# Performance work log

Hardware: AMD Instinct MI355X
Metric: run time of the kernel (lower is better)

The kernel has to match this reference:

```python
import jax, jax.numpy as jnp
import numpy as np

LAMBDA_SCALE = 0.5
EPS = 1e-6

def setup_inputs() -> dict:
    key = jax.random.key(0)
    ks = jax.random.split(key, 9)
    B, S, D, E, F = 4, 2048, 1024, 8, 4096
    x = jax.random.normal(ks[0], (B, S, D), dtype=jnp.float32)
    prev_logits = jax.random.normal(ks[1], (B, S, E), dtype=jnp.float32)
    # router params (nn.Linear default init scale ~ 1/sqrt(fan_in))
    Wt = jax.random.normal(ks[2], (E, D), dtype=jnp.float32) / np.sqrt(D)
    Wgt = jax.random.normal(ks[3], (E, E), dtype=jnp.float32) / np.sqrt(E)
    We_logits = jnp.zeros((E,), dtype=jnp.float32)
    # expert MLPs, stacked over the expert axis
    W1 = jax.random.normal(ks[4], (E, D, F), dtype=jnp.float32) / np.sqrt(D)
    b1 = jax.random.normal(ks[5], (E, F), dtype=jnp.float32) * 0.01
    W2 = jax.random.normal(ks[6], (E, F, D), dtype=jnp.float32) / np.sqrt(F)
    b2 = jax.random.normal(ks[7], (E, D), dtype=jnp.float32) * 0.01
    return {"x": x, "prev_logits": prev_logits, "Wt": Wt, "Wgt": Wgt,
            "We_logits": We_logits, "W1": W1, "b1": b1, "W2": W2, "b2": b2}

def reference(x, prev_logits, Wt, Wgt, We_logits, W1, b1, W2, b2):
    # router logits: [B,S,E]
    logits = jnp.einsum('bsd,ed->bse', x, Wt) + jnp.einsum('bse,fe->bsf', prev_logits, Wgt)
    st = jax.nn.softmax(logits, axis=-1)
    We = jax.nn.sigmoid(We_logits)                      # [E]
    mask = (st > LAMBDA_SCALE * We).astype(st.dtype)    # data-dependent gate mask
    g = st * mask                                       # [B,S,E]
    # dense per-expert MLP over all tokens (faithful to the module)
    h = jax.nn.gelu(jnp.einsum('bsd,edf->bsef', x, W1) + b1, approximate=False)  # [B,S,E,F]
    outk = jnp.einsum('bsef,efd->bsed', h, W2) + b2     # [B,S,E,D]
    y = jnp.einsum('bse,bsed->bsd', g, outk)
    y = y / (jnp.sum(g, axis=-1, keepdims=True) + EPS)
    return (y, jax.lax.stop_gradient(logits))
```

## Files before the change

kernel.cpp:

```cpp
#include <hip/hip_runtime.h>
#include <math.h>

#define NTOK 8192
#define DDIM 1024
#define NEXP 8
#define FDIM 4096
#define MAXROWS 25600

typedef short bf16x8 __attribute__((ext_vector_type(8)));
typedef float f32x4 __attribute__((ext_vector_type(4)));

#define BAR() asm volatile("s_barrier" ::: "memory")
#define WAITVL0() asm volatile("s_waitcnt vmcnt(0) lgkmcnt(0)" ::: "memory")

static __device__ __forceinline__ unsigned short f2bf(float f) {
  unsigned int u = __float_as_uint(f);
  u += 0x7fffu + ((u >> 16) & 1u);
  return (unsigned short)(u >> 16);
}

static __device__ __forceinline__ void gl_lds16(const void* g, void* l) {
  __builtin_amdgcn_global_load_lds(
      (const __attribute__((address_space(1))) unsigned int*)g,
      (__attribute__((address_space(3))) unsigned int*)l, 16, 0, 0);
}

static __device__ __forceinline__ float gelu_f(float v) {
  float x2 = v * v;
  float p = fmaf(x2, 0.10294422f, 2.3021183f);
  float E = __builtin_amdgcn_exp2f(v * p);
  return v - v * __builtin_amdgcn_rcpf(E + 1.f);
}

__global__ __launch_bounds__(256) void router_kernel(
    const float* __restrict__ x, const float* __restrict__ prev,
    const float* __restrict__ Wt, const float* __restrict__ Wgt,
    const float* __restrict__ Wel,
    float* __restrict__ gn, float* __restrict__ logits_out)
{
  __shared__ float wt_s[NEXP * DDIM];
  const int tid = threadIdx.x;
  for (int i = tid; i < NEXP * DDIM; i += 256) wt_s[i] = Wt[i];
  __syncthreads();
  const int lane = tid & 63;
  const int t = blockIdx.x * 4 + (tid >> 6);

  const float* xr = x + (size_t)t * DDIM;
  float acc[NEXP];
#pragma unroll
  for (int e = 0; e < NEXP; ++e) acc[e] = 0.f;
  for (int k = lane; k < DDIM; k += 64) {
    float xv = xr[k];
#pragma unroll
    for (int e = 0; e < NEXP; ++e) acc[e] += xv * wt_s[e * DDIM + k];
  }
#pragma unroll
  for (int e = 0; e < NEXP; ++e) {
    float v = acc[e];
#pragma unroll
    for (int off = 32; off >= 1; off >>= 1) v += __shfl_xor(v, off);
    acc[e] = v;
  }
  float pl[NEXP];
#pragma unroll
  for (int e = 0; e < NEXP; ++e) pl[e] = prev[(size_t)t * NEXP + e];
#pragma unroll
  for (int e = 0; e < NEXP; ++e) {
    float s = acc[e];
#pragma unroll
    for (int e2 = 0; e2 < NEXP; ++e2) s += pl[e2] * Wgt[e * NEXP + e2];
    acc[e] = s;
  }
  float mx = acc[0];
#pragma unroll
  for (int e = 1; e < NEXP; ++e) mx = fmaxf(mx, acc[e]);
  float st[NEXP]; float se = 0.f;
#pragma unroll
  for (int e = 0; e < NEXP; ++e) { st[e] = expf(acc[e] - mx); se += st[e]; }
  float inv = 1.f / se;
  float g[NEXP]; float gs = 0.f;
#pragma unroll
  for (int e = 0; e < NEXP; ++e) {
    float s = st[e] * inv;
    float we = 1.f / (1.f + expf(-Wel[e]));
    float gg = (s > 0.5f * we) ? s : 0.f;
    g[e] = gg; gs += gg;
  }
  float r = 1.f / (gs + 1e-6f);
  if (lane < NEXP) {
    gn[(size_t)t * NEXP + lane] = g[lane] * r;
    logits_out[(size_t)t * NEXP + lane] = acc[lane];
  }
}

__global__ __launch_bounds__(256) void cast_kernel(
    const float* __restrict__ in, unsigned short* __restrict__ out)
{
  size_t i = ((size_t)blockIdx.x * 256 + threadIdx.x) * 8;
  float4 a = *(const float4*)(in + i);
  float4 b = *(const float4*)(in + i + 4);
  unsigned short tb[8];
  tb[0]=f2bf(a.x); tb[1]=f2bf(a.y); tb[2]=f2bf(a.z); tb[3]=f2bf(a.w);
  tb[4]=f2bf(b.x); tb[5]=f2bf(b.y); tb[6]=f2bf(b.z); tb[7]=f2bf(b.w);
  *(uint4*)(out + i) = *(const uint4*)tb;
}

__global__ __launch_bounds__(256) void count_kernel(
    const float* __restrict__ gn, int* __restrict__ cnt)
{
  const int e = blockIdx.x, tid = threadIdx.x;
  int c = 0;
  for (int t = tid; t < NTOK; t += 256) c += (gn[(size_t)t * NEXP + e] > 0.f) ? 1 : 0;
#pragma unroll
  for (int o = 32; o >= 1; o >>= 1) c += __shfl_xor(c, o);
  __shared__ int sm[4];
  if ((tid & 63) == 0) sm[tid >> 6] = c;
  __syncthreads();
  if (tid == 0) cnt[e] = sm[0] + sm[1] + sm[2] + sm[3];
}

__global__ __launch_bounds__(256) void compact_kernel(
    const float* __restrict__ gn, const int* __restrict__ cnt,
    int* __restrict__ offs, int* __restrict__ rowtok, int* __restrict__ rowof)
{
  const int e = blockIdx.x, tid = threadIdx.x;
  int base = 0;
#pragma unroll
  for (int q = 0; q < 8; ++q) if (q < e) base += (cnt[q] + 127) & ~127;
  const int padcnt = (cnt[e] + 127) & ~127;
  if (e == 0 && tid == 0) {
    int a = 0; offs[0] = 0;
#pragma unroll
    for (int q = 0; q < 8; ++q) { a += (cnt[q] + 127) & ~127; offs[q + 1] = a; }
  }
  __shared__ int wsm[4];
  __shared__ int running;
  if (tid == 0) running = 0;
  __syncthreads();
  const int lane = tid & 63, wv = tid >> 6;
  for (int c0 = 0; c0 < NTOK; c0 += 256) {
    const int t = c0 + tid;
    const bool pr = gn[(size_t)t * NEXP + e] > 0.f;
    unsigned long long bal = __ballot(pr);
    int pre = __popcll(bal & ((1ull << lane) - 1ull));
    if (lane == 0) wsm[wv] = __popcll(bal);
    __syncthreads();
    int wbase = 0;
#pragma unroll
    for (int q = 0; q < 4; ++q) if (q < wv) wbase += wsm[q];
    const int tot = wsm[0] + wsm[1] + wsm[2] + wsm[3];
    const int idx = base + running + wbase + pre;
    if (pr) rowtok[idx] = t;
    rowof[(size_t)t * NEXP + e] = pr ? idx : -1;
    __syncthreads();
    if (tid == 0) running += tot;
  }
  __syncthreads();
  for (int i = cnt[e] + tid; i < padcnt; i += 256) rowtok[base + i] = -1;
}

__global__ __launch_bounds__(256) void y_init_kernel(
    const float* __restrict__ gn, const float* __restrict__ b2,
    float* __restrict__ y)
{
  const int t = blockIdx.y;
  const int d = blockIdx.x * 256 + threadIdx.x;
  float s = 0.f;
#pragma unroll
  for (int e = 0; e < NEXP; ++e) s += gn[(size_t)t * NEXP + e] * b2[(size_t)e * DDIM + d];
  y[(size_t)t * DDIM + d] = s;
}

__global__ __launch_bounds__(256) void transcvt(
    const float* __restrict__ in, unsigned short* __restrict__ out,
    int Kin, int Nin)
{
  __shared__ float tile[64][65];
  const size_t zo = (size_t)blockIdx.z * Kin * Nin;
  const float* inp = in + zo;
  unsigned short* outp = out + zo;
  const int k0 = blockIdx.y * 64, n0 = blockIdx.x * 64;
  const int tid = threadIdx.x;
  const int r = tid >> 4, c4 = (tid & 15) * 4;
#pragma unroll
  for (int rr = 0; rr < 64; rr += 16) {
    float4 v = *(const float4*)(inp + (size_t)(k0 + r + rr) * Nin + n0 + c4);
    tile[r + rr][c4] = v.x; tile[r + rr][c4 + 1] = v.y;
    tile[r + rr][c4 + 2] = v.z; tile[r + rr][c4 + 3] = v.w;
  }
  __syncthreads();
#pragma unroll
  for (int it = 0; it < 2; ++it) {
    const int o = it * 256 + tid;
    const int n = o >> 3, ks = (o & 7) * 8;
    unsigned short tb[8];
#pragma unroll
    for (int j = 0; j < 8; ++j) tb[j] = f2bf(tile[ks + j][n]);
    *(uint4*)(outp + (size_t)(n0 + n) * Kin + k0 + ks) = *(const uint4*)tb;
  }
}


__global__ __launch_bounds__(128, 2) void gemm_h(
    const unsigned short* __restrict__ xb,
    const unsigned short* __restrict__ W,
    size_t wstride,
    const float* __restrict__ b1,
    const float* __restrict__ gn,
    const int* __restrict__ rowtok,
    const int* __restrict__ offs,
    int efix,
    unsigned short* __restrict__ hb)
{
  __shared__ unsigned short As[2][4096];
  __shared__ unsigned short Bs[2][4096];
  __shared__ float gns[128];
  __shared__ float b1s[128];
  __shared__ int toks[128];
  const int tid = threadIdx.x;

  int mt, e, hbase;
  if (efix >= 0) {
    e = efix;
    hbase = offs[e];
    mt = (hbase >> 7) + blockIdx.y;
    if (mt * 128 >= offs[e + 1]) return;
  } else {
    mt = blockIdx.y;
    const int r0 = mt * 128;
    if (r0 >= offs[8]) return;
    e = 0;
#pragma unroll
    for (int q = 1; q < 8; ++q) if (r0 >= offs[q]) e = q;
    hbase = 0;
  }
  const int n0 = blockIdx.x * 128;
  const unsigned short* We = W + (size_t)e * wstride;

  {
    const int tk = rowtok[mt * 128 + tid];
    toks[tid] = tk;
    gns[tid] = (tk >= 0) ? gn[(size_t)tk * NEXP + e] : 0.f;
    b1s[tid] = b1[(size_t)e * FDIM + n0 + tid];
  }
  __syncthreads();

  const int st_row = tid >> 2;
  const int st_off = (((tid & 3) ^ (st_row & 3)) << 3);
  const unsigned short* aP[4];
  const unsigned short* bP[4];
#pragma unroll
  for (int i = 0; i < 4; ++i) {
    int tk = toks[i * 32 + st_row]; if (tk < 0) tk = 0;
    aP[i] = xb + (size_t)tk * DDIM + st_off;
    bP[i] = We + (size_t)(n0 + i * 32 + st_row) * DDIM + st_off;
  }
  const int ldst = tid * 8;

  const int lane = tid & 63;
  const int w = tid >> 6;
  const int fr = lane & 15;
  const int rdoff = (((lane >> 4) ^ (lane & 3)) << 3);

  f32x4 acc[8][4];
#pragma unroll
  for (int i = 0; i < 8; ++i)
#pragma unroll
    for (int j = 0; j < 4; ++j) acc[i][j] = (f32x4){0.f, 0.f, 0.f, 0.f};

  auto stage = [&](int kt, int b) {
    const int ke = kt * 32;
#pragma unroll
    for (int i = 0; i < 4; ++i) {
      gl_lds16(aP[i] + ke, &As[b][i * 1024 + ldst]);
      gl_lds16(bP[i] + ke, &Bs[b][i * 1024 + ldst]);
    }
  };

  const int NT = DDIM / 32;
  stage(0, 0);
  WAITVL0(); BAR();

  for (int t = 0; t < NT; ++t) {
    const int cur = t & 1;
    if (t + 1 < NT) stage(t + 1, cur ^ 1);
    bf16x8 af[8], bfv[4];
#pragma unroll
    for (int i = 0; i < 8; ++i)
      af[i] = *(const bf16x8*)&As[cur][(i * 16 + fr) * 32 + rdoff];
#pragma unroll
    for (int j = 0; j < 4; ++j)
      bfv[j] = *(const bf16x8*)&Bs[cur][(w * 64 + j * 16 + fr) * 32 + rdoff];
#pragma unroll
    for (int i = 0; i < 8; ++i)
#pragma unroll
      for (int j = 0; j < 4; ++j)
        acc[i][j] = __builtin_amdgcn_mfma_f32_16x16x32_bf16(af[i], bfv[j], acc[i][j], 0, 0, 0);
    if (t + 1 < NT) { WAITVL0(); BAR(); }
  }

#pragma unroll
  for (int i = 0; i < 8; ++i)
#pragma unroll
    for (int r = 0; r < 4; ++r) {
      const int row = i * 16 + (lane >> 4) * 4 + r;
      const int tk = toks[row];
      if (tk < 0) continue;
      const float gv = gns[row];
      unsigned short* hrow = hb + (size_t)(mt * 128 + row - hbase) * FDIM + n0;
#pragma unroll
      for (int j = 0; j < 4; ++j) {
        const int col = w * 64 + j * 16 + fr;
        float v = gelu_f(acc[i][j][r] + b1s[col]) * gv;
        hrow[col] = f2bf(v);
      }
    }
}

__global__ __launch_bounds__(128, 2) void gemm_o(
    const unsigned short* __restrict__ hb,
    const unsigned short* __restrict__ W,
    size_t wstride,
    const int* __restrict__ rowtok,
    const int* __restrict__ offs,
    int efix,
    float* __restrict__ yout,
    int mode)
{
  __shared__ unsigned short As[2][4096];
  __shared__ unsigned short Bs[2][4096];
  __shared__ int toks[128];
  const int tid = threadIdx.x;

  int mt, e, hbase;
  if (efix >= 0) {
    e = efix;
    hbase = offs[e];
    mt = (hbase >> 7) + blockIdx.y;
    if (mt * 128 >= offs[e + 1]) return;
  } else {
    mt = blockIdx.y;
    const int r0 = mt * 128;
    if (r0 >= offs[8]) return;
    e = 0;
#pragma unroll
    for (int q = 1; q < 8; ++q) if (r0 >= offs[q]) e = q;
    hbase = 0;
  }
  const int n0 = blockIdx.x * 128;
  const unsigned short* We = W + (size_t)e * wstride;

  toks[tid] = rowtok[mt * 128 + tid];
  __syncthreads();

  const int st_row = tid >> 2;
  const int st_off = (((tid & 3) ^ (st_row & 3)) << 3);
  const unsigned short* aP[4];
  const unsigned short* bP[4];
#pragma unroll
  for (int i = 0; i < 4; ++i) {
    aP[i] = hb + (size_t)(mt * 128 - hbase + i * 32 + st_row) * FDIM + st_off;
    bP[i] = We + (size_t)(n0 + i * 32 + st_row) * FDIM + st_off;
  }
  const int ldst = tid * 8;

  const int lane = tid & 63;
  const int w = tid >> 6;
  const int fr = lane & 15;
  const int rdoff = (((lane >> 4) ^ (lane & 3)) << 3);

  f32x4 acc[8][4];
#pragma unroll
  for (int i = 0; i < 8; ++i)
#pragma unroll
    for (int j = 0; j < 4; ++j) acc[i][j] = (f32x4){0.f, 0.f, 0.f, 0.f};

  auto stage = [&](int kt, int b) {
    const int ke = kt * 32;
#pragma unroll
    for (int i = 0; i < 4; ++i) {
      gl_lds16(aP[i] + ke, &As[b][i * 1024 + ldst]);
      gl_lds16(bP[i] + ke, &Bs[b][i * 1024 + ldst]);
    }
  };

  const int NT = FDIM / 32;
  stage(0, 0);
  WAITVL0(); BAR();

  for (int t = 0; t < NT; ++t) {
    const int cur = t & 1;
    if (t + 1 < NT) stage(t + 1, cur ^ 1);
    bf16x8 af[8], bfv[4];
#pragma unroll
    for (int i = 0; i < 8; ++i)
      af[i] = *(const bf16x8*)&As[cur][(i * 16 + fr) * 32 + rdoff];
#pragma unroll
    for (int j = 0; j < 4; ++j)
      bfv[j] = *(const bf16x8*)&Bs[cur][(w * 64 + j * 16 + fr) * 32 + rdoff];
#pragma unroll
    for (int i = 0; i < 8; ++i)
#pragma unroll
      for (int j = 0; j < 4; ++j)
        acc[i][j] = __builtin_amdgcn_mfma_f32_16x16x32_bf16(af[i], bfv[j], acc[i][j], 0, 0, 0);
    if (t + 1 < NT) { WAITVL0(); BAR(); }
  }

#pragma unroll
  for (int i = 0; i < 8; ++i)
#pragma unroll
    for (int r = 0; r < 4; ++r) {
      const int row = i * 16 + (lane >> 4) * 4 + r;
      if (mode == 0) {
        const int tk = toks[row];
        if (tk < 0) continue;
        float* yrow = yout + (size_t)tk * DDIM + n0;
#pragma unroll
        for (int j = 0; j < 4; ++j) {
          const int col = w * 64 + j * 16 + fr;
          yrow[col] += acc[i][j][r];
        }
      } else {
        float* yrow = yout + (size_t)(mt * 128 + row) * DDIM + n0;
#pragma unroll
        for (int j = 0; j < 4; ++j) {
          const int col = w * 64 + j * 16 + fr;
          yrow[col] = acc[i][j][r];
        }
      }
    }
}

__global__ __launch_bounds__(256) void combine_kernel(
    const float* __restrict__ hb2, const int* __restrict__ rowof,
    const float* __restrict__ gn, const float* __restrict__ b2,
    float* __restrict__ y)
{
  const int t = blockIdx.y;
  const int d = blockIdx.x * 256 + threadIdx.x;
  float s = 0.f;
#pragma unroll
  for (int e = 0; e < NEXP; ++e) {
    s += gn[(size_t)t * NEXP + e] * b2[(size_t)e * DDIM + d];
    const int r = rowof[(size_t)t * NEXP + e];
    if (r >= 0) s += hb2[(size_t)r * DDIM + d];
  }
  y[(size_t)t * DDIM + d] = s;
}

extern "C" void kernel_launch(void* const* d_in, const int* in_sizes, int n_in,
                              void* d_out, int out_size, void* d_ws, size_t ws_size,
                              hipStream_t stream) {
  (void)in_sizes; (void)n_in; (void)out_size;
  const float* x    = (const float*)d_in[0];
  const float* prev = (const float*)d_in[1];
  const float* Wt   = (const float*)d_in[2];
  const float* Wgt  = (const float*)d_in[3];
  const float* Wel  = (const float*)d_in[4];
  const float* W1   = (const float*)d_in[5];
  const float* b1   = (const float*)d_in[6];
  const float* W2   = (const float*)d_in[7];
  const float* b2   = (const float*)d_in[8];

  float* y      = (float*)d_out;
  float* logits = y + (size_t)NTOK * DDIM;

  char* ws = (char*)d_ws;
  size_t pos = 0;
  auto take = [&](size_t bytes) -> char* {
    char* r = ws + pos; pos += (bytes + 255) & ~(size_t)255; return r;
  };
  float* gn            = (float*)take((size_t)NTOK * NEXP * 4);
  int* cnt             = (int*)take(64);
  int* offs            = (int*)take(64);
  int* rowtok          = (int*)take((size_t)MAXROWS * 4);
  int* rowof           = (int*)take((size_t)NTOK * NEXP * 4);
  unsigned short* xb   = (unsigned short*)take((size_t)NTOK * DDIM * 2);
  const size_t fixed = pos;

  const size_t wexp = (size_t)FDIM * DDIM;
  const size_t needA = fixed + 2 * NEXP * wexp * 2 + (size_t)MAXROWS * FDIM * 2
                       + (size_t)MAXROWS * DDIM * 4 + 4096;
  const bool tierA = ws_size >= needA;

  router_kernel<<<dim3(NTOK / 4), dim3(256), 0, stream>>>(x, prev, Wt, Wgt, Wel, gn, logits);
  cast_kernel<<<dim3((NTOK * DDIM) / (8 * 256)), dim3(256), 0, stream>>>(x, xb);
  count_kernel<<<dim3(NEXP), dim3(256), 0, stream>>>(gn, cnt);
  compact_kernel<<<dim3(NEXP), dim3(256), 0, stream>>>(gn, cnt, offs, rowtok, rowof);

  if (tierA) {
    unsigned short* W1b = (unsigned short*)take(NEXP * wexp * 2);
    unsigned short* W2b = (unsigned short*)take(NEXP * wexp * 2);
    unsigned short* hb  = (unsigned short*)take((size_t)MAXROWS * FDIM * 2);
    float* hb2          = (float*)take((size_t)MAXROWS * DDIM * 4);

    transcvt<<<dim3(FDIM / 64, DDIM / 64, NEXP), dim3(256), 0, stream>>>(W1, W1b, DDIM, FDIM);
    transcvt<<<dim3(DDIM / 64, FDIM / 64, NEXP), dim3(256), 0, stream>>>(W2, W2b, FDIM, DDIM);
    gemm_h<<<dim3(FDIM / 128, MAXROWS / 128), dim3(128), 0, stream>>>(
        xb, W1b, wexp, b1, gn, rowtok, offs, -1, hb);
    gemm_o<<<dim3(DDIM / 128, MAXROWS / 128), dim3(128), 0, stream>>>(
        hb, W2b, wexp, rowtok, offs, -1, hb2, 1);
    combine_kernel<<<dim3(DDIM / 256, NTOK), dim3(256), 0, stream>>>(hb2, rowof, gn, b2, y);
  } else {
    unsigned short* Wb = (unsigned short*)take(wexp * 2);
    unsigned short* hb = (unsigned short*)take((size_t)NTOK * FDIM * 2);

    y_init_kernel<<<dim3(DDIM / 256, NTOK), dim3(256), 0, stream>>>(gn, b2, y);
    for (int e = 0; e < NEXP; ++e) {
      transcvt<<<dim3(FDIM / 64, DDIM / 64, 1), dim3(256), 0, stream>>>(
          W1 + (size_t)e * wexp, Wb, DDIM, FDIM);
      gemm_h<<<dim3(FDIM / 128, 64), dim3(128), 0, stream>>>(
          xb, Wb, 0, b1, gn, rowtok, offs, e, hb);
      transcvt<<<dim3(DDIM / 64, FDIM / 64, 1), dim3(256), 0, stream>>>(
          W2 + (size_t)e * wexp, Wb, FDIM, DDIM);
      gemm_o<<<dim3(DDIM / 128, 64), dim3(128), 0, stream>>>(
          hb, Wb, 0, rowtok, offs, e, y, 0);
    }
  }
}
```

Before: 546.4 us.

## Use 256x256-tile, 512-thread grouped GEMMs with interleaved prefetch and bf16 expert outputs

Replaces the 128x128 grouped expert GEMMs on the main path with 256x256 tiles, K=64 steps and 8 waves. Global-to-LDS loads for the next tile are split into chunks interleaved with MFMA groups, using partial vmcnt waits and s_setprio. Expert padding goes to 256 rows to match the new tiles. The second GEMM's per-expert outputs are stored as bf16 instead of fp32, halving intermediate traffic for the combine step. This raises per-block LDS and register use, adds padded rows, and loses some precision in the intermediate outputs.

Measured after the change: 500.9 us, median of 3. 1.09x faster.

```diff
diff --git a/kernel.cpp b/kernel.cpp
--- a/kernel.cpp
+++ b/kernel.cpp
@@ -5,18 +5,21 @@
 #define DDIM 1024
 #define NEXP 8
 #define FDIM 4096
-#define MAXROWS 25600
+#define MAXROWS 26624
 
 typedef short bf16x8 __attribute__((ext_vector_type(8)));
 typedef float f32x4 __attribute__((ext_vector_type(4)));
 
 #define BAR() asm volatile("s_barrier" ::: "memory")
-#define WAITVL0() asm volatile("s_waitcnt vmcnt(0) lgkmcnt(0)" ::: "memory")
+#define WAITV(n) asm volatile("s_waitcnt vmcnt(" #n ")" ::: "memory")
 
 static __device__ __forceinline__ unsigned short f2bf(float f) {
   unsigned int u = __float_as_uint(f);
   u += 0x7fffu + ((u >> 16) & 1u);
   return (unsigned short)(u >> 16);
+}
+static __device__ __forceinline__ float bf2f(unsigned short b) {
+  return __uint_as_float(((unsigned int)b) << 16);
 }
 
 static __device__ __forceinline__ void gl_lds16(const void* g, void* l) {
@@ -126,12 +129,12 @@
   const int e = blockIdx.x, tid = threadIdx.x;
   int base = 0;
 #pragma unroll
-  for (int q = 0; q < 8; ++q) if (q < e) base += (cnt[q] + 127) & ~127;
-  const int padcnt = (cnt[e] + 127) & ~127;
+  for (int q = 0; q < 8; ++q) if (q < e) base += (cnt[q] + 255) & ~255;
+  const int padcnt = (cnt[e] + 255) & ~255;
   if (e == 0 && tid == 0) {
     int a = 0; offs[0] = 0;
 #pragma unroll
-    for (int q = 0; q < 8; ++q) { a += (cnt[q] + 127) & ~127; offs[q + 1] = a; }
+    for (int q = 0; q < 8; ++q) { a += (cnt[q] + 255) & ~255; offs[q + 1] = a; }
   }
   __shared__ int wsm[4];
   __shared__ int running;
@@ -201,10 +204,362 @@
 }
 
 
-__global__ __launch_bounds__(128, 2) void gemm_h(
+__global__ __launch_bounds__(512, 2) void gemm_h256(
     const unsigned short* __restrict__ xb,
     const unsigned short* __restrict__ W,
-    size_t wstride,
+    const float* __restrict__ b1,
+    const float* __restrict__ gn,
+    const int* __restrict__ rowtok,
+    const int* __restrict__ offs,
+    unsigned short* __restrict__ hb)
+{
+  __shared__ unsigned short As[2][256 * 64];
+  __shared__ unsigned short Bs[2][256 * 64];
+  __shared__ float gns[256];
+  __shared__ float b1s[256];
+  __shared__ int toks[256];
+  const int tid = threadIdx.x;
+  const int r0 = blockIdx.y * 256;
+  if (r0 >= offs[8]) return;
+  int e = 0;
+#pragma unroll
+  for (int q = 1; q < 8; ++q) if (r0 >= offs[q]) e = q;
+  const int n0 = blockIdx.x * 256;
+  const unsigned short* We = W + (size_t)e * FDIM * DDIM;
+
+  if (tid < 256) {
+    const int tk = rowtok[r0 + tid];
+    toks[tid] = tk;
+    gns[tid] = (tk >= 0) ? gn[(size_t)tk * NEXP + e] : 0.f;
+    b1s[tid] = b1[(size_t)e * FDIM + n0 + tid];
+  }
+  __syncthreads();
+
+  const int rc = tid >> 3;
+  const int gld = tid & 7;
+  const int gsrc = gld ^ (rc & 7);
+  const unsigned short* aP[4];
+  const unsigned short* bP[4];
+#pragma unroll
+  for (int c = 0; c < 4; ++c) {
+    int tk = toks[c * 64 + rc]; if (tk < 0) tk = 0;
+    aP[c] = xb + (size_t)tk * DDIM + gsrc * 8;
+    bP[c] = We + (size_t)(n0 + c * 64 + rc) * DDIM + gsrc * 8;
+  }
+
+  const int lane = tid & 63;
+  const int wid = tid >> 6;
+  const int wm = (wid >> 2) * 128;
+  const int wn = (wid & 3) * 64;
+  const int fr = lane & 15;
+  const int q4 = lane >> 4;
+
+  f32x4 acc[8][4];
+#pragma unroll
+  for (int i = 0; i < 8; ++i)
+#pragma unroll
+    for (int j = 0; j < 4; ++j) acc[i][j] = (f32x4){0.f, 0.f, 0.f, 0.f};
+
+  auto stA = [&](int kt, int b, int c) { gl_lds16(aP[c] + kt * 64, &As[b][c * 4096 + tid * 8]); };
+  auto stB = [&](int kt, int b, int c) { gl_lds16(bP[c] + kt * 64, &Bs[b][c * 4096 + tid * 8]); };
+  auto rdA = [&](int cur, int i, int kk) -> bf16x8 {
+    const int row = wm + i * 16 + fr;
+    const int sl = (kk * 4 + q4) ^ (row & 7);
+    return *(const bf16x8*)&As[cur][row * 64 + sl * 8];
+  };
+  auto rdB = [&](int cur, int j, int kk) -> bf16x8 {
+    const int row = wn + j * 16 + fr;
+    const int sl = (kk * 4 + q4) ^ (row & 7);
+    return *(const bf16x8*)&Bs[cur][row * 64 + sl * 8];
+  };
+
+  const int NT = DDIM / 64;
+  bf16x8 aX[4][2], aY[4][2], bb[2][2];
+
+#pragma unroll
+  for (int c = 0; c < 4; ++c) { stA(0, 0, c); stB(0, 0, c); }
+  WAITV(0); BAR();
+
+  for (int t = 0; t < NT - 1; ++t) {
+    const int cur = t & 1, nxt = cur ^ 1;
+    stA(t + 1, nxt, 0); stA(t + 1, nxt, 1);
+    WAITV(2); BAR();
+#pragma unroll
+    for (int i = 0; i < 4; ++i) { aX[i][0] = rdA(cur, i, 0); aX[i][1] = rdA(cur, i, 1); }
+#pragma unroll
+    for (int j = 0; j < 2; ++j) { bb[j][0] = rdB(cur, j, 0); bb[j][1] = rdB(cur, j, 1); }
+    __builtin_amdgcn_s_setprio(1);
+#pragma unroll
+    for (int i = 0; i < 4; ++i)
+#pragma unroll
+      for (int j = 0; j < 2; ++j)
+#pragma unroll
+        for (int kk = 0; kk < 2; ++kk)
+          acc[i][j] = __builtin_amdgcn_mfma_f32_16x16x32_bf16(aX[i][kk], bb[j][kk], acc[i][j], 0, 0, 0);
+    __builtin_amdgcn_s_setprio(0);
+    stA(t + 1, nxt, 2); stA(t + 1, nxt, 3);
+#pragma unroll
+    for (int i = 0; i < 4; ++i) { aY[i][0] = rdA(cur, 4 + i, 0); aY[i][1] = rdA(cur, 4 + i, 1); }
+    __builtin_amdgcn_s_setprio(1);
+#pragma unroll
+    for (int i = 0; i < 4; ++i)
+#pragma unroll
+      for (int j = 0; j < 2; ++j)
+#pragma unroll
+        for (int kk = 0; kk < 2; ++kk)
+          acc[4 + i][j] = __builtin_amdgcn_mfma_f32_16x16x32_bf16(aY[i][kk], bb[j][kk], acc[4 + i][j], 0, 0, 0);
+    __builtin_amdgcn_s_setprio(0);
+    stB(t + 1, nxt, 0); stB(t + 1, nxt, 1);
+#pragma unroll
+    for (int j = 0; j < 2; ++j) { bb[j][0] = rdB(cur, 2 + j, 0); bb[j][1] = rdB(cur, 2 + j, 1); }
+    __builtin_amdgcn_s_setprio(1);
+#pragma unroll
+    for (int i = 0; i < 4; ++i)
+#pragma unroll
+      for (int j = 0; j < 2; ++j)
+#pragma unroll
+        for (int kk = 0; kk < 2; ++kk)
+          acc[4 + i][2 + j] = __builtin_amdgcn_mfma_f32_16x16x32_bf16(aY[i][kk], bb[j][kk], acc[4 + i][2 + j], 0, 0, 0);
+    __builtin_amdgcn_s_setprio(0);
+    stB(t + 1, nxt, 2); stB(t + 1, nxt, 3);
+    __builtin_amdgcn_s_setprio(1);
+#pragma unroll
+    for (int i = 0; i < 4; ++i)
+#pragma unroll
+      for (int j = 0; j < 2; ++j)
+#pragma unroll
+        for (int kk = 0; kk < 2; ++kk)
+          acc[i][2 + j] = __builtin_amdgcn_mfma_f32_16x16x32_bf16(aX[i][kk], bb[j][kk], acc[i][2 + j], 0, 0, 0);
+    __builtin_amdgcn_s_setprio(0);
+    BAR();
+  }
+  {
+    const int cur = (NT - 1) & 1;
+    WAITV(0); BAR();
+#pragma unroll
+    for (int i = 0; i < 4; ++i) { aX[i][0] = rdA(cur, i, 0); aX[i][1] = rdA(cur, i, 1); }
+#pragma unroll
+    for (int i = 0; i < 4; ++i) { aY[i][0] = rdA(cur, 4 + i, 0); aY[i][1] = rdA(cur, 4 + i, 1); }
+#pragma unroll
+    for (int j = 0; j < 2; ++j) { bb[j][0] = rdB(cur, j, 0); bb[j][1] = rdB(cur, j, 1); }
+#pragma unroll
+    for (int i = 0; i < 4; ++i)
+#pragma unroll
+      for (int j = 0; j < 2; ++j)
+#pragma unroll
+        for (int kk = 0; kk < 2; ++kk) {
+          acc[i][j] = __builtin_amdgcn_mfma_f32_16x16x32_bf16(aX[i][kk], bb[j][kk], acc[i][j], 0, 0, 0);
+          acc[4 + i][j] = __builtin_amdgcn_mfma_f32_16x16x32_bf16(aY[i][kk], bb[j][kk], acc[4 + i][j], 0, 0, 0);
+        }
+#pragma unroll
+    for (int j = 0; j < 2; ++j) { bb[j][0] = rdB(cur, 2 + j, 0); bb[j][1] = rdB(cur, 2 + j, 1); }
+#pragma unroll
+    for (int i = 0; i < 4; ++i)
+#pragma unroll
+      for (int j = 0; j < 2; ++j)
+#pragma unroll
+        for (int kk = 0; kk < 2; ++kk) {
+          acc[i][2 + j] = __builtin_amdgcn_mfma_f32_16x16x32_bf16(aX[i][kk], bb[j][kk], acc[i][2 + j], 0, 0, 0);
+          acc[4 + i][2 + j] = __builtin_amdgcn_mfma_f32_16x16x32_bf16(aY[i][kk], bb[j][kk], acc[4 + i][2 + j], 0, 0, 0);
+        }
+  }
+
+#pragma unroll
+  for (int i = 0; i < 8; ++i)
+#pragma unroll
+    for (int rr = 0; rr < 4; ++rr) {
+      const int row = wm + i * 16 + q4 * 4 + rr;
+      const int tk = toks[row];
+      if (tk < 0) continue;
+      const float gv = gns[row];
+      unsigned short* hrow = hb + (size_t)(r0 + row) * FDIM + n0;
+#pragma unroll
+      for (int j = 0; j < 4; ++j) {
+        const int col = wn + j * 16 + fr;
+        hrow[col] = f2bf(gelu_f(acc[i][j][rr] + b1s[col]) * gv);
+      }
+    }
+}
+
+__global__ __launch_bounds__(512, 2) void gemm_o256(
+    const unsigned short* __restrict__ hb,
+    const unsigned short* __restrict__ W,
+    const int* __restrict__ offs,
+    unsigned short* __restrict__ hb2)
+{
+  __shared__ unsigned short As[2][256 * 64];
+  __shared__ unsigned short Bs[2][256 * 64];
+  const int tid = threadIdx.x;
+  const int r0 = blockIdx.y * 256;
+  if (r0 >= offs[8]) return;
+  int e = 0;
+#pragma unroll
+  for (int q = 1; q < 8; ++q) if (r0 >= offs[q]) e = q;
+  const int n0 = blockIdx.x * 256;
+  const unsigned short* We = W + (size_t)e * FDIM * DDIM;
+
+  const int rc = tid >> 3;
+  const int gld = tid & 7;
+  const int gsrc = gld ^ (rc & 7);
+  const unsigned short* aP[4];
+  const unsigned short* bP[4];
+#pragma unroll
+  for (int c = 0; c < 4; ++c) {
+    aP[c] = hb + (size_t)(r0 + c * 64 + rc) * FDIM + gsrc * 8;
+    bP[c] = We + (size_t)(n0 + c * 64 + rc) * FDIM + gsrc * 8;
+  }
+
+  const int lane = tid & 63;
+  const int wid = tid >> 6;
+  const int wm = (wid >> 2) * 128;
+  const int wn = (wid & 3) * 64;
+  const int fr = lane & 15;
+  const int q4 = lane >> 4;
+
+  f32x4 acc[8][4];
+#pragma unroll
+  for (int i = 0; i < 8; ++i)
+#pragma unroll
+    for (int j = 0; j < 4; ++j) acc[i][j] = (f32x4){0.f, 0.f, 0.f, 0.f};
+
+  auto stA = [&](int kt, int b, int c) { gl_lds16(aP[c] + kt * 64, &As[b][c * 4096 + tid * 8]); };
+  auto stB = [&](int kt, int b, int c) { gl_lds16(bP[c] + kt * 64, &Bs[b][c * 4096 + tid * 8]); };
+  auto rdA = [&](int cur, int i, int kk) -> bf16x8 {
+    const int row = wm + i * 16 + fr;
+    const int sl = (kk * 4 + q4) ^ (row & 7);
+    return *(const bf16x8*)&As[cur][row * 64 + sl * 8];
+  };
+  auto rdB = [&](int cur, int j, int kk) -> bf16x8 {
+    const int row = wn + j * 16 + fr;
+    const int sl = (kk * 4 + q4) ^ (row & 7);
+    return *(const bf16x8*)&Bs[cur][row * 64 + sl * 8];
+  };
+
+  const int NT = FDIM / 64;
+  bf16x8 aX[4][2], aY[4][2], bb[2][2];
+
+#pragma unroll
+  for (int c = 0; c < 4; ++c) { stA(0, 0, c); stB(0, 0, c); }
+  WAITV(0); BAR();
+
+  for (int t = 0; t < NT - 1; ++t) {
+    const int cur = t & 1, nxt = cur ^ 1;
+    stA(t + 1, nxt, 0); stA(t + 1, nxt, 1);
+    WAITV(2); BAR();
+#pragma unroll
+    for (int i = 0; i < 4; ++i) { aX[i][0] = rdA(cur, i, 0); aX[i][1] = rdA(cur, i, 1); }
+#pragma unroll
+    for (int j = 0; j < 2; ++j) { bb[j][0] = rdB(cur, j, 0); bb[j][1] = rdB(cur, j, 1); }
+    __builtin_amdgcn_s_setprio(1);
+#pragma unroll
+    for (int i = 0; i < 4; ++i)
+#pragma unroll
+      for (int j = 0; j < 2; ++j)
+#pragma unroll
+        for (int kk = 0; kk < 2; ++kk)
+          acc[i][j] = __builtin_amdgcn_mfma_f32_16x16x32_bf16(aX[i][kk], bb[j][kk], acc[i][j], 0, 0, 0);
+    __builtin_amdgcn_s_setprio(0);
+    stA(t + 1, nxt, 2); stA(t + 1, nxt, 3);
+#pragma unroll
+    for (int i = 0; i < 4; ++i) { aY[i][0] = rdA(cur, 4 + i, 0); aY[i][1] = rdA(cur, 4 + i, 1); }
+    __builtin_amdgcn_s_setprio(1);
+#pragma unroll
+    for (int i = 0; i < 4; ++i)
+#pragma unroll
+      for (int j = 0; j < 2; ++j)
+#pragma unroll
+        for (int kk = 0; kk < 2; ++kk)
+          acc[4 + i][j] = __builtin_amdgcn_mfma_f32_16x16x32_bf16(aY[i][kk], bb[j][kk], acc[4 + i][j], 0, 0, 0);
+    __builtin_amdgcn_s_setprio(0);
+    stB(t + 1, nxt, 0); stB(t + 1, nxt, 1);
+#pragma unroll
+    for (int j = 0; j < 2; ++j) { bb[j][0] = rdB(cur, 2 + j, 0); bb[j][1] = rdB(cur, 2 + j, 1); }
+    __builtin_amdgcn_s_setprio(1);
+#pragma unroll
+    for (int i = 0; i < 4; ++i)
+#pragma unroll
+      for (int j = 0; j < 2; ++j)
+#pragma unroll
+        for (int kk = 0; kk < 2; ++kk)
+          acc[4 + i][2 + j] = __builtin_amdgcn_mfma_f32_16x16x32_bf16(aY[i][kk], bb[j][kk], acc[4 + i][2 + j], 0, 0, 0);
+    __builtin_amdgcn_s_setprio(0);
+    stB(t + 1, nxt, 2); stB(t + 1, nxt, 3);
+    __builtin_amdgcn_s_setprio(1);
+#pragma unroll
+    for (int i = 0; i < 4; ++i)
+#pragma unroll
+      for (int j = 0; j < 2; ++j)
+#pragma unroll
+        for (int kk = 0; kk < 2; ++kk)
+          acc[i][2 + j] = __builtin_amdgcn_mfma_f32_16x16x32_bf16(aX[i][kk], bb[j][kk], acc[i][2 + j], 0, 0, 0);
+    __builtin_amdgcn_s_setprio(0);
+    BAR();
+  }
+  {
+    const int cur = (NT - 1) & 1;
+    WAITV(0); BAR();
+#pragma unroll
+    for (int i = 0; i < 4; ++i) { aX[i][0] = rdA(cur, i, 0); aX[i][1] = rdA(cur, i, 1); }
+#pragma unroll
+    for (int i = 0; i < 4; ++i) { aY[i][0] = rdA(cur, 4 + i, 0); aY[i][1] = rdA(cur, 4 + i, 1); }
+#pragma unroll
+    for (int j = 0; j < 2; ++j) { bb[j][0] = rdB(cur, j, 0); bb[j][1] = rdB(cur, j, 1); }
+#pragma unroll
+    for (int i = 0; i < 4; ++i)
+#pragma unroll
+      for (int j = 0; j < 2; ++j)
+#pragma unroll
+        for (int kk = 0; kk < 2; ++kk) {
+          acc[i][j] = __builtin_amdgcn_mfma_f32_16x16x32_bf16(aX[i][kk], bb[j][kk], acc[i][j], 0, 0, 0);
+          acc[4 + i][j] = __builtin_amdgcn_mfma_f32_16x16x32_bf16(aY[i][kk], bb[j][kk], acc[4 + i][j], 0, 0, 0);
+        }
+#pragma unroll
+    for (int j = 0; j < 2; ++j) { bb[j][0] = rdB(cur, 2 + j, 0); bb[j][1] = rdB(cur, 2 + j, 1); }
+#pragma unroll
+    for (int i = 0; i < 4; ++i)
+#pragma unroll
+      for (int j = 0; j < 2; ++j)
+#pragma unroll
+        for (int kk = 0; kk < 2; ++kk) {
+          acc[i][2 + j] = __builtin_amdgcn_mfma_f32_16x16x32_bf16(aX[i][kk], bb[j][kk], acc[i][2 + j], 0, 0, 0);
+          acc[4 + i][2 + j] = __builtin_amdgcn_mfma_f32_16x16x32_bf16(aY[i][kk], bb[j][kk], acc[4 + i][2 + j], 0, 0, 0);
+        }
+  }
+
+#pragma unroll
+  for (int i = 0; i < 8; ++i)
+#pragma unroll
+    for (int rr = 0; rr < 4; ++rr) {
+      const int row = wm + i * 16 + q4 * 4 + rr;
+      unsigned short* orow = hb2 + (size_t)(r0 + row) * DDIM + n0;
+#pragma unroll
+      for (int j = 0; j < 4; ++j) {
+        const int col = wn + j * 16 + fr;
+        orow[col] = f2bf(acc[i][j][rr]);
+      }
+    }
+}
+
+__global__ __launch_bounds__(256) void combine_kernel(
+    const unsigned short* __restrict__ hb2, const int* __restrict__ rowof,
+    const float* __restrict__ gn, const float* __restrict__ b2,
+    float* __restrict__ y)
+{
+  const int t = blockIdx.y;
+  const int d = blockIdx.x * 256 + threadIdx.x;
+  float s = 0.f;
+#pragma unroll
+  for (int e = 0; e < NEXP; ++e) {
+    s += gn[(size_t)t * NEXP + e] * b2[(size_t)e * DDIM + d];
+    const int r = rowof[(size_t)t * NEXP + e];
+    if (r >= 0) s += bf2f(hb2[(size_t)r * DDIM + d]);
+  }
+  y[(size_t)t * DDIM + d] = s;
+}
+
+__global__ __launch_bounds__(128, 2) void gemm_h128(
+    const unsigned short* __restrict__ xb,
+    const unsigned short* __restrict__ W,
     const float* __restrict__ b1,
     const float* __restrict__ gn,
     const int* __restrict__ rowtok,
@@ -218,24 +573,12 @@
   __shared__ float b1s[128];
   __shared__ int toks[128];
   const int tid = threadIdx.x;
-
-  int mt, e, hbase;
-  if (efix >= 0) {
-    e = efix;
-    hbase = offs[e];
-    mt = (hbase >> 7) + blockIdx.y;
-    if (mt * 128 >= offs[e + 1]) return;
-  } else {
-    mt = blockIdx.y;
-    const int r0 = mt * 128;
-    if (r0 >= offs[8]) return;
-    e = 0;
-#pragma unroll
-    for (int q = 1; q < 8; ++q) if (r0 >= offs[q]) e = q;
-    hbase = 0;
-  }
+  const int e = efix;
+  const int hbase = offs[e];
+  const int mt = (hbase >> 7) + blockIdx.y;
+  if (mt * 128 >= offs[e + 1]) return;
   const int n0 = blockIdx.x * 128;
-  const unsigned short* We = W + (size_t)e * wstride;
+  const unsigned short* We = W;
 
   {
     const int tk = rowtok[mt * 128 + tid];
@@ -256,7 +599,6 @@
     bP[i] = We + (size_t)(n0 + i * 32 + st_row) * DDIM + st_off;
   }
   const int ldst = tid * 8;
-
   const int lane = tid & 63;
   const int w = tid >> 6;
   const int fr = lane & 15;
@@ -279,26 +621,22 @@
 
   const int NT = DDIM / 32;
   stage(0, 0);
-  WAITVL0(); BAR();
-
+  asm volatile("s_waitcnt vmcnt(0) lgkmcnt(0)" ::: "memory"); BAR();
   for (int t = 0; t < NT; ++t) {
     const int cur = t & 1;
     if (t + 1 < NT) stage(t + 1, cur ^ 1);
     bf16x8 af[8], bfv[4];
 #pragma unroll
-    for (int i = 0; i < 8; ++i)
-      af[i] = *(const bf16x8*)&As[cur][(i * 16 + fr) * 32 + rdoff];
-#pragma unroll
-    for (int j = 0; j < 4; ++j)
-      bfv[j] = *(const bf16x8*)&Bs[cur][(w * 64 + j * 16 + fr) * 32 + rdoff];
+    for (int i = 0; i < 8; ++i) af[i] = *(const bf16x8*)&As[cur][(i * 16 + fr) * 32 + rdoff];
+#pragma unroll
+    for (int j = 0; j < 4; ++j) bfv[j] = *(const bf16x8*)&Bs[cur][(w * 64 + j * 16 + fr) * 32 + rdoff];
 #pragma unroll
     for (int i = 0; i < 8; ++i)
 #pragma unroll
       for (int j = 0; j < 4; ++j)
         acc[i][j] = __builtin_amdgcn_mfma_f32_16x16x32_bf16(af[i], bfv[j], acc[i][j], 0, 0, 0);
-    if (t + 1 < NT) { WAITVL0(); BAR(); }
-  }
-
+    if (t + 1 < NT) { asm volatile("s_waitcnt vmcnt(0) lgkmcnt(0)" ::: "memory"); BAR(); }
+  }
 #pragma unroll
   for (int i = 0; i < 8; ++i)
 #pragma unroll
@@ -311,44 +649,28 @@
 #pragma unroll
       for (int j = 0; j < 4; ++j) {
         const int col = w * 64 + j * 16 + fr;
-        float v = gelu_f(acc[i][j][r] + b1s[col]) * gv;
-        hrow[col] = f2bf(v);
+        hrow[col] = f2bf(gelu_f(acc[i][j][r] + b1s[col]) * gv);
       }
     }
 }
 
-__global__ __launch_bounds__(128, 2) void gemm_o(
+__global__ __launch_bounds__(128, 2) void gemm_o128(
     const unsigned short* __restrict__ hb,
     const unsigned short* __restrict__ W,
-    size_t wstride,
     const int* __restrict__ rowtok,
     const int* __restrict__ offs,
     int efix,
-    float* __restrict__ yout,
-    int mode)
+    float* __restrict__ yout)
 {
   __shared__ unsigned short As[2][4096];
   __shared__ unsigned short Bs[2][4096];
   __shared__ int toks[128];
   const int tid = threadIdx.x;
-
-  int mt, e, hbase;
-  if (efix >= 0) {
-    e = efix;
-    hbase = offs[e];
-    mt = (hbase >> 7) + blockIdx.y;
-    if (mt * 128 >= offs[e + 1]) return;
-  } else {
-    mt = blockIdx.y;
-    const int r0 = mt * 128;
-    if (r0 >= offs[8]) return;
-    e = 0;
-#pragma unroll
-    for (int q = 1; q < 8; ++q) if (r0 >= offs[q]) e = q;
-    hbase = 0;
-  }
+  const int e = efix;
+  const int hbase = offs[e];
+  const int mt = (hbase >> 7) + blockIdx.y;
+  if (mt * 128 >= offs[e + 1]) return;
   const int n0 = blockIdx.x * 128;
-  const unsigned short* We = W + (size_t)e * wstride;
 
   toks[tid] = rowtok[mt * 128 + tid];
   __syncthreads();
@@ -360,10 +682,9 @@
 #pragma unroll
   for (int i = 0; i < 4; ++i) {
     aP[i] = hb + (size_t)(mt * 128 - hbase + i * 32 + st_row) * FDIM + st_off;
-    bP[i] = We + (size_t)(n0 + i * 32 + st_row) * FDIM + st_off;
+    bP[i] = W + (size_t)(n0 + i * 32 + st_row) * FDIM + st_off;
   }
   const int ldst = tid * 8;
-
   const int lane = tid & 63;
   const int w = tid >> 6;
   const int fr = lane & 15;
@@ -386,66 +707,36 @@
 
   const int NT = FDIM / 32;
   stage(0, 0);
-  WAITVL0(); BAR();
-
+  asm volatile("s_waitcnt vmcnt(0) lgkmcnt(0)" ::: "memory"); BAR();
   for (int t = 0; t < NT; ++t) {
     const int cur = t & 1;
     if (t + 1 < NT) stage(t + 1, cur ^ 1);
     bf16x8 af[8], bfv[4];
 #pragma unroll
-    for (int i = 0; i < 8; ++i)
-      af[i] = *(const bf16x8*)&As[cur][(i * 16 + fr) * 32 + rdoff];
-#pragma unroll
-    for (int j = 0; j < 4; ++j)
-      bfv[j] = *(const bf16x8*)&Bs[cur][(w * 64 + j * 16 + fr) * 32 + rdoff];
+    for (int i = 0; i < 8; ++i) af[i] = *(const bf16x8*)&As[cur][(i * 16 + fr) * 32 + rdoff];
+#pragma unroll
+    for (int j = 0; j < 4; ++j) bfv[j] = *(const bf16x8*)&Bs[cur][(w * 64 + j * 16 + fr) * 32 + rdoff];
 #pragma unroll
     for (int i = 0; i < 8; ++i)
 #pragma unroll
       for (int j = 0; j < 4; ++j)
         acc[i][j] = __builtin_amdgcn_mfma_f32_16x16x32_bf16(af[i], bfv[j], acc[i][j], 0, 0, 0);
-    if (t + 1 < NT) { WAITVL0(); BAR(); }
-  }
-
+    if (t + 1 < NT) { asm volatile("s_waitcnt vmcnt(0) lgkmcnt(0)" ::: "memory"); BAR(); }
+  }
 #pragma unroll
   for (int i = 0; i < 8; ++i)
 #pragma unroll
     for (int r = 0; r < 4; ++r) {
       const int row = i * 16 + (lane >> 4) * 4 + r;
-      if (mode == 0) {
-        const int tk = toks[row];
-        if (tk < 0) continue;
-        float* yrow = yout + (size_t)tk * DDIM + n0;
-#pragma unroll
-        for (int j = 0; j < 4; ++j) {
-          const int col = w * 64 + j * 16 + fr;
-          yrow[col] += acc[i][j][r];
-        }
-      } else {
-        float* yrow = yout + (size_t)(mt * 128 + row) * DDIM + n0;
-#pragma unroll
-        for (int j = 0; j < 4; ++j) {
-          const int col = w * 64 + j * 16 + fr;
-          yrow[col] = acc[i][j][r];
-        }
+      const int tk = toks[row];
+      if (tk < 0) continue;
+      float* yrow = yout + (size_t)tk * DDIM + n0;
+#pragma unroll
+      for (int j = 0; j < 4; ++j) {
+        const int col = w * 64 + j * 16 + fr;
+        yrow[col] += acc[i][j][r];
       }
     }
-}
-
-__global__ __launch_bounds__(256) void combine_kernel(
-    const float* __restrict__ hb2, const int* __restrict__ rowof,
-    const float* __restrict__ gn, const float* __restrict__ b2,
-    float* __restrict__ y)
-{
-  const int t = blockIdx.y;
-  const int d = blockIdx.x * 256 + threadIdx.x;
-  float s = 0.f;
-#pragma unroll
-  for (int e = 0; e < NEXP; ++e) {
-    s += gn[(size_t)t * NEXP + e] * b2[(size_t)e * DDIM + d];
-    const int r = rowof[(size_t)t * NEXP + e];
-    if (r >= 0) s += hb2[(size_t)r * DDIM + d];
-  }
-  y[(size_t)t * DDIM + d] = s;
 }
 
 extern "C" void kernel_launch(void* const* d_in, const int* in_sizes, int n_in,
@@ -480,7 +771,7 @@
 
   const size_t wexp = (size_t)FDIM * DDIM;
   const size_t needA = fixed + 2 * NEXP * wexp * 2 + (size_t)MAXROWS * FDIM * 2
-                       + (size_t)MAXROWS * DDIM * 4 + 4096;
+                       + (size_t)MAXROWS * DDIM * 2 + 4096;
   const bool tierA = ws_size >= needA;
 
   router_kernel<<<dim3(NTOK / 4), dim3(256), 0, stream>>>(x, prev, Wt, Wgt, Wel, gn, logits);
@@ -492,14 +783,14 @@
     unsigned short* W1b = (unsigned short*)take(NEXP * wexp * 2);
     unsigned short* W2b = (unsigned short*)take(NEXP * wexp * 2);
     unsigned short* hb  = (unsigned short*)take((size_t)MAXROWS * FDIM * 2);
-    float* hb2          = (float*)take((size_t)MAXROWS * DDIM * 4);
+    unsigned short* hb2 = (unsigned short*)take((size_t)MAXROWS * DDIM * 2);
 
     transcvt<<<dim3(FDIM / 64, DDIM / 64, NEXP), dim3(256), 0, stream>>>(W1, W1b, DDIM, FDIM);
     transcvt<<<dim3(DDIM / 64, FDIM / 64, NEXP), dim3(256), 0, stream>>>(W2, W2b, FDIM, DDIM);
-    gemm_h<<<dim3(FDIM / 128, MAXROWS / 128), dim3(128), 0, stream>>>(
-        xb, W1b, wexp, b1, gn, rowtok, offs, -1, hb);
-    gemm_o<<<dim3(DDIM / 128, MAXROWS / 128), dim3(128), 0, stream>>>(
-        hb, W2b, wexp, rowtok, offs, -1, hb2, 1);
+    gemm_h256<<<dim3(FDIM / 256, MAXROWS / 256), dim3(512), 0, stream>>>(
+        xb, W1b, b1, gn, rowtok, offs, hb);
+    gemm_o256<<<dim3(DDIM / 256, MAXROWS / 256), dim3(512), 0, stream>>>(
+        hb, W2b, offs, hb2);
     combine_kernel<<<dim3(DDIM / 256, NTOK), dim3(256), 0, stream>>>(hb2, rowof, gn, b2, y);
   } else {
     unsigned short* Wb = (unsigned short*)take(wexp * 2);
@@ -509,12 +800,12 @@
     for (int e = 0; e < NEXP; ++e) {
       transcvt<<<dim3(FDIM / 64, DDIM / 64, 1), dim3(256), 0, stream>>>(
           W1 + (size_t)e * wexp, Wb, DDIM, FDIM);
-      gemm_h<<<dim3(FDIM / 128, 64), dim3(128), 0, stream>>>(
-          xb, Wb, 0, b1, gn, rowtok, offs, e, hb);
+      gemm_h128<<<dim3(FDIM / 128, 64), dim3(128), 0, stream>>>(
+          xb, Wb, b1, gn, rowtok, offs, e, hb);
       transcvt<<<dim3(DDIM / 64, FDIM / 64, 1), dim3(256), 0, stream>>>(
           W2 + (size_t)e * wexp, Wb, FDIM, DDIM);
-      gemm_o<<<dim3(DDIM / 128, 64), dim3(128), 0, stream>>>(
-          hb, Wb, 0, rowtok, offs, e, y, 0);
+      gemm_o128<<<dim3(DDIM / 128, 64), dim3(128), 0, stream>>>(
+          hb, Wb, rowtok, offs, e, y);
     }
   }
 }
```
